# Optimization experiments

Measured on AMD Instinct MI355X. Metric: run time of the kernel, lower is better.

The kernel has to match this reference:

```python
import jax, jax.numpy as jnp
import numpy as np

N_NODES = 100000
N_EDGES = 1600000
N_ETYPES = 3
IN_FEATS = 128
HEADS = 4
OUT_FEATS = 16
EDGE_FEATS = 64
NEG_SLOPE = 0.2


def setup_inputs() -> dict:
    key = jax.random.key(0)
    ks = jax.random.split(key, 10)
    return {
        "x": jax.random.normal(ks[0], (N_NODES, IN_FEATS), jnp.float32),
        "W": jax.random.normal(ks[1], (IN_FEATS, HEADS * OUT_FEATS), jnp.float32) * 0.05,
        "W_e": jax.random.normal(ks[2], (EDGE_FEATS, HEADS * EDGE_FEATS), jnp.float32) * 0.05,
        "attn_l": jax.random.normal(ks[3], (HEADS, OUT_FEATS), jnp.float32) * 0.1,
        "attn_r": jax.random.normal(ks[4], (HEADS, OUT_FEATS), jnp.float32) * 0.1,
        "attn_e": jax.random.normal(ks[5], (HEADS, EDGE_FEATS), jnp.float32) * 0.1,
        "edge_emb": jax.random.normal(ks[6], (N_ETYPES, EDGE_FEATS), jnp.float32),
        "src": jax.random.randint(ks[7], (N_EDGES,), 0, N_NODES, jnp.int32),
        "dst": jax.random.randint(ks[8], (N_EDGES,), 0, N_NODES, jnp.int32),
        "etype": jax.random.randint(ks[9], (N_EDGES,), 0, N_ETYPES, jnp.int32),
    }


def reference(x, W, W_e, attn_l, attn_r, attn_e, edge_emb, src, dst, etype):
    N = x.shape[0]
    H, D = attn_l.shape
    # node projection: [N, H, D]
    feat = (x @ W).reshape(N, H, D)
    # per-node attention halves: [N, H]
    el = jnp.einsum("nhd,hd->nh", feat, attn_l)
    er = jnp.einsum("nhd,hd->nh", feat, attn_r)
    # per-etype edge term: [T, H]
    e_feat = (edge_emb @ W_e).reshape(edge_emb.shape[0], H, -1)
    ee = jnp.einsum("the,he->th", e_feat, attn_e)
    # per-edge pre-softmax score: [E, H]
    s = el[src] + er[dst] + ee[etype]
    s = jnp.where(s > 0, s, NEG_SLOPE * s)  # leaky_relu
    # edge softmax over incoming edges of each dst node (homogeneous graph)
    m = jax.ops.segment_max(s, dst, num_segments=N)
    e = jnp.exp(s - m[dst])
    z = jax.ops.segment_sum(e, dst, num_segments=N)
    a = e / z[dst]  # [E, H]
    # u_mul_e + sum aggregation: [N, H, D]
    msg = feat[src] * a[:, :, None]
    rst = jax.ops.segment_sum(msg, dst, num_segments=N)
    return rst, a
```

## Files before the change

kernel.cpp:

```cpp
#include <hip/hip_runtime.h>
#include <hip/hip_bf16.h>

#define N_NODES   100000
#define N_EDGES   1600000
#define N_ETYPES  3
#define IN_FEATS  128
#define HEADS     4
#define OUT_FEATS 16
#define EDGE_FEATS 64
#define HD        64
#define NEG_SLOPE 0.2f
#define MAXD_LDS  128

#define NBUCK     800
#define NPB       125
#define PBLK      400
#define EPB       4000
#define BCAP      2560
#define FROWS     32
#define NFEAT     (N_NODES / FROWS)
#define WTROWS    80


typedef short s16x8 __attribute__((ext_vector_type(8)));
typedef float f32x4 __attribute__((ext_vector_type(4)));

__device__ __forceinline__ short f2bs(float f) {
    __hip_bfloat16 h = __float2bfloat16(f);
    return *reinterpret_cast<short*>(&h);
}

__global__ __launch_bounds__(256) void wt_prep_kernel(
    const float* __restrict__ W,
    const float* __restrict__ attn_l,
    const float* __restrict__ attn_r,
    short* __restrict__ WTb, int* __restrict__ cnt)
{
    const int t = blockIdx.x * 256 + threadIdx.x;
    const int n = t >> 7, k = t & 127;
    short v;
    if (n < 64) {
        v = f2bs(W[k * HD + n]);
    } else if (n < 72) {
        const int h = (n - 64) & 3;
        const float* av = (n < 68) ? attn_l : attn_r;
        float s = 0.f;
#pragma unroll
        for (int d = 0; d < OUT_FEATS; ++d)
            s += W[k * HD + h * OUT_FEATS + d] * av[h * OUT_FEATS + d];
        v = f2bs(s);
    } else {
        v = 0;
    }
    WTb[n * IN_FEATS + k] = v;
    if (blockIdx.x == 0)
        for (int j = threadIdx.x; j < NBUCK; j += 256) cnt[j] = 0;
}

#define XS_STRIDE 136
__global__ __launch_bounds__(320) void feat_scatter_kernel(
    const float* __restrict__ x,
    const short* __restrict__ WTb,
    const float* __restrict__ edge_emb,
    const float* __restrict__ W_e,
    const float* __restrict__ attn_e,
    const int* __restrict__ src, const int* __restrict__ dst,
    const int* __restrict__ etype,
    __hip_bfloat16* __restrict__ featb,
    float* __restrict__ el,
    float* __restrict__ er,
    float* __restrict__ ee,
    int* __restrict__ cnt, int2* __restrict__ sc_bucket)
{
    __shared__ __align__(16) char smem[FROWS * XS_STRIDE * 2];
    const int t = threadIdx.x;
    const int b = blockIdx.x;

    if (b < PBLK) {
        int* h = (int*)smem;
        int buld[13];
        for (int j = t; j < NBUCK; j += 320) h[j] = 0;
        __syncthreads();
        const int e0 = b * EPB;
        int k = 0;
        for (int i = t; i < EPB; i += 320, ++k) {
            const int dn = dst[e0 + i];
            const int bu = dn / NPB;
            const int ld = dn - bu * NPB;
            buld[k] = bu | (ld << 16);
            atomicAdd(&h[bu], 1);
        }
        __syncthreads();
        for (int j = t; j < NBUCK; j += 320) {
            const int c = h[j];
            h[j] = j * BCAP + (c ? atomicAdd(&cnt[j], c) : 0);
        }
        __syncthreads();
        k = 0;
        for (int i = t; i < EPB; i += 320, ++k) {
            const int e  = e0 + i;
            const int bu = buld[k] & 0xFFFF;
            const int ld = buld[k] >> 16;
            const int slot = atomicAdd(&h[bu], 1);
            sc_bucket[slot] = make_int2(src[e], e | (etype[e] << 21) | (ld << 23));
        }
        return;
    }

    if (b == PBLK) {
        const int wv = t >> 6, e = t & 63;
        for (int j = wv; j < N_ETYPES * HEADS; j += 5) {
            const int ty = j >> 2, h = j & 3;
            float ef = 0.f;
#pragma unroll
            for (int k = 0; k < EDGE_FEATS; ++k)
                ef += edge_emb[ty * EDGE_FEATS + k] *
                      W_e[k * (HEADS * EDGE_FEATS) + h * EDGE_FEATS + e];
            float v = ef * attn_e[h * EDGE_FEATS + e];
#pragma unroll
            for (int m = 1; m < 64; m <<= 1) v += __shfl_xor(v, m, 64);
            if (e == 0) ee[ty * HEADS + h] = v;
        }
        return;
    }

    short* Xs = (short*)smem;
    const int row0 = (b - PBLK - 1) * FROWS;
    if (t < 256) {
        const int r = t >> 3, k0 = (t & 7) * 16;
        const float4* xg = (const float4*)(x + (size_t)(row0 + r) * IN_FEATS + k0);
        const float4 v0 = xg[0], v1 = xg[1], v2 = xg[2], v3 = xg[3];
        s16x8 p0, p1;
        p0[0] = f2bs(v0.x); p0[1] = f2bs(v0.y); p0[2] = f2bs(v0.z); p0[3] = f2bs(v0.w);
        p0[4] = f2bs(v1.x); p0[5] = f2bs(v1.y); p0[6] = f2bs(v1.z); p0[7] = f2bs(v1.w);
        p1[0] = f2bs(v2.x); p1[1] = f2bs(v2.y); p1[2] = f2bs(v2.z); p1[3] = f2bs(v2.w);
        p1[4] = f2bs(v3.x); p1[5] = f2bs(v3.y); p1[6] = f2bs(v3.z); p1[7] = f2bs(v3.w);
        *(s16x8*)&Xs[r * XS_STRIDE + k0]     = p0;
        *(s16x8*)&Xs[r * XS_STRIDE + k0 + 8] = p1;
    }

    const int w    = t >> 6;
    const int lane = t & 63;
    const int m    = lane & 15;
    const int q    = lane >> 4;

    s16x8 bfr[4];
#pragma unroll
    for (int kb = 0; kb < 4; ++kb)
        bfr[kb] = *(const s16x8*)(WTb + (size_t)(w * 16 + m) * IN_FEATS + kb * 32 + q * 8);

    __syncthreads();

#pragma unroll
    for (int rg = 0; rg < 2; ++rg) {
        f32x4 acc = {0.f, 0.f, 0.f, 0.f};
#pragma unroll
        for (int kb = 0; kb < 4; ++kb) {
            const s16x8 af = *(const s16x8*)&Xs[(rg * 16 + m) * XS_STRIDE + kb * 32 + q * 8];
            acc = __builtin_amdgcn_mfma_f32_16x16x32_bf16(af, bfr[kb], acc, 0, 0, 0);
        }
        if (w < 4) {
#pragma unroll
            for (int r = 0; r < 4; ++r) {
                const int row = row0 + rg * 16 + q * 4 + r;
                featb[(size_t)row * HD + w * 16 + m] = __float2bfloat16(acc[r]);
            }
        } else {
#pragma unroll
            for (int r = 0; r < 4; ++r) {
                const int row = row0 + rg * 16 + q * 4 + r;
                if (m < 4)      el[row * HEADS + m]       = acc[r];
                else if (m < 8) er[row * HEADS + (m - 4)] = acc[r];
            }
        }
    }
}

__global__ __launch_bounds__(256) void bucket_csr_kernel(
    int2* __restrict__ sc_bucket, const int* __restrict__ cnt,
    int* __restrict__ ptr, int* __restrict__ deg)
{
    __shared__ int2 sbuf[BCAP];
    __shared__ int sdeg4[4][128];
    __shared__ int sdg[128];
    __shared__ int scur[128];
    const int t = threadIdx.x, b = blockIdx.x;
    const int wid = t >> 6;

    sdeg4[0][t & 127] = 0; sdeg4[1][t & 127] = 0;
    if (t < 128) { sdeg4[2][t] = 0; sdeg4[3][t] = 0; }
    __syncthreads();
    const int count = min(cnt[b], BCAP);
    const int base  = b * BCAP;

    for (int i = t; i < count; i += 256) {
        const int2 v = sc_bucket[base + i];
        sbuf[i] = v;
        atomicAdd(&sdeg4[wid][(v.y >> 23) & 0x7F], 1);
    }
    __syncthreads();
    int orig = 0;
    if (t < 128) {
        orig = sdeg4[0][t] + sdeg4[1][t] + sdeg4[2][t] + sdeg4[3][t];
        sdg[t] = orig;
    }
    __syncthreads();
    for (int off = 1; off < 128; off <<= 1) {
        const int v = (t < 128 && t >= off) ? sdg[t - off] : 0;
        __syncthreads();
        if (t < 128) sdg[t] += v;
        __syncthreads();
    }
    if (t < 128) {
        const int excl = sdg[t] - orig;
        if (t < NPB) {
            ptr[b * NPB + t] = base + excl;
            deg[b * NPB + t] = orig;
        }
        scur[t] = base + excl;
    }
    __syncthreads();
    for (int i = t; i < count; i += 256) {
        const int2 v = sbuf[i];
        const int ld = (v.y >> 23) & 0x7F;
        const int slot = atomicAdd(&scur[ld], 1);
        sc_bucket[slot] = make_int2(v.x, v.y & 0x7FFFFF);
    }
}

__global__ __launch_bounds__(256) void agg_kernel(
    const int2* __restrict__ sc_csr, const int* __restrict__ ptr,
    const int* __restrict__ deg_arr,
    const float* __restrict__ el, const float* __restrict__ er,
    const float* __restrict__ ee, const __hip_bfloat16* __restrict__ featb,
    float* __restrict__ rst, float* __restrict__ a_out)
{
    __shared__ float w_lds[4][MAXD_LDS * HEADS];
    __shared__ int   s_lds[4][MAXD_LDS];
    __shared__ int   e_lds[4][MAXD_LDS];
    const int wid  = threadIdx.x >> 6;
    const int lane = threadIdx.x & 63;
    const int n    = blockIdx.x * 4 + wid;

    const int p0  = ptr[n];
    const int deg = deg_arr[n];
    float* wl = w_lds[wid];
    int*   sl = s_lds[wid];
    int*   elds = e_lds[wid];
    const ushort* fb = (const ushort*)featb;

    if (deg <= MAXD_LDS) {
        const int eo = lane >> 2;
        const int hA = lane & 3;
        const float er_n = er[n * HEADS + hA];
        const float g0 = ee[hA], g1 = ee[HEADS + hA], g2 = ee[2 * HEADS + hA];

        float zacc = 0.f;
        for (int i0 = 0; i0 < deg; i0 += 32) {
            const int idxA = i0 + eo;
            const int idxB = i0 + 16 + eo;
            const bool pA = idxA < deg;
            const bool pB = idxB < deg;
            int2 vA = make_int2(0, 0), vB = make_int2(0, 0);
            if (pA) vA = sc_csr[p0 + idxA];
            if (pB) vB = sc_csr[p0 + idxB];
            float eA = 0.f, eB = 0.f;
            if (pA) eA = el[vA.x * HEADS + hA];
            if (pB) eB = el[vB.x * HEADS + hA];
            if (pA) {
                const int ty = vA.y >> 21;
                float s = eA + er_n + ((ty == 0) ? g0 : ((ty == 1) ? g1 : g2));
                s = s > 0.f ? s : NEG_SLOPE * s;
                const float w = __expf(s);
                wl[idxA * HEADS + hA] = w;
                if (hA == 0) sl[idxA] = vA.x;
                if (hA == 1) elds[idxA] = vA.y & 0x1FFFFF;
                zacc += w;
            }
            if (pB) {
                const int ty = vB.y >> 21;
                float s = eB + er_n + ((ty == 0) ? g0 : ((ty == 1) ? g1 : g2));
                s = s > 0.f ? s : NEG_SLOPE * s;
                const float w = __expf(s);
                wl[idxB * HEADS + hA] = w;
                if (hA == 0) sl[idxB] = vB.x;
                if (hA == 1) elds[idxB] = vB.y & 0x1FFFFF;
                zacc += w;
            }
        }
        zacc += __shfl_xor(zacc, 4, 64);
        zacc += __shfl_xor(zacc, 8, 64);
        zacc += __shfl_xor(zacc, 16, 64);
        zacc += __shfl_xor(zacc, 32, 64);
        const float izA = (deg > 0) ? __frcp_rn(zacc) : 0.f;

        for (int idx = eo; idx < deg; idx += 16)
            a_out[((size_t)elds[idx] << 2) + hA] = wl[idx * HEADS + hA] * izA;

        const int q8 = lane >> 3;
        const int c8 = lane & 7;
        const int h8 = c8 >> 1;
        const float inv_z = (deg > 0) ? __frcp_rn(__shfl(zacc, h8, 64)) : 0.f;

        float a0 = 0.f, a1 = 0.f, a2 = 0.f, a3 = 0.f;
        float a4 = 0.f, a5 = 0.f, a6 = 0.f, a7 = 0.f;
        int i = 0;
        for (; i + 16 <= deg; i += 16) {
            const int idxA = i + q8, idxB = i + 8 + q8;
            const int sA = sl[idxA], sB = sl[idxB];
            const float wA = wl[idxA * HEADS + h8];
            const float wB = wl[idxB * HEADS + h8];
            const uint4 fA = *(const uint4*)(fb + ((size_t)sA << 6) + (c8 << 3));
            const uint4 fB = *(const uint4*)(fb + ((size_t)sB << 6) + (c8 << 3));
            a0 += __uint_as_float(fA.x << 16) * wA;
            a1 += __uint_as_float(fA.x & 0xFFFF0000u) * wA;
            a2 += __uint_as_float(fA.y << 16) * wA;
            a3 += __uint_as_float(fA.y & 0xFFFF0000u) * wA;
            a4 += __uint_as_float(fA.z << 16) * wA;
            a5 += __uint_as_float(fA.z & 0xFFFF0000u) * wA;
            a6 += __uint_as_float(fA.w << 16) * wA;
            a7 += __uint_as_float(fA.w & 0xFFFF0000u) * wA;
            a0 += __uint_as_float(fB.x << 16) * wB;
            a1 += __uint_as_float(fB.x & 0xFFFF0000u) * wB;
            a2 += __uint_as_float(fB.y << 16) * wB;
            a3 += __uint_as_float(fB.y & 0xFFFF0000u) * wB;
            a4 += __uint_as_float(fB.z << 16) * wB;
            a5 += __uint_as_float(fB.z & 0xFFFF0000u) * wB;
            a6 += __uint_as_float(fB.w << 16) * wB;
            a7 += __uint_as_float(fB.w & 0xFFFF0000u) * wB;
        }
        if (i + 8 <= deg) {
            const int idx = i + q8;
            const int sA = sl[idx];
            const float wA = wl[idx * HEADS + h8];
            const uint4 fA = *(const uint4*)(fb + ((size_t)sA << 6) + (c8 << 3));
            a0 += __uint_as_float(fA.x << 16) * wA;
            a1 += __uint_as_float(fA.x & 0xFFFF0000u) * wA;
            a2 += __uint_as_float(fA.y << 16) * wA;
            a3 += __uint_as_float(fA.y & 0xFFFF0000u) * wA;
            a4 += __uint_as_float(fA.z << 16) * wA;
            a5 += __uint_as_float(fA.z & 0xFFFF0000u) * wA;
            a6 += __uint_as_float(fA.w << 16) * wA;
            a7 += __uint_as_float(fA.w & 0xFFFF0000u) * wA;
            i += 8;
        }
        if (i + q8 < deg) {
            const int idx = i + q8;
            const int sA = sl[idx];
            const float wA = wl[idx * HEADS + h8];
            const uint4 fA = *(const uint4*)(fb + ((size_t)sA << 6) + (c8 << 3));
            a0 += __uint_as_float(fA.x << 16) * wA;
            a1 += __uint_as_float(fA.x & 0xFFFF0000u) * wA;
            a2 += __uint_as_float(fA.y << 16) * wA;
            a3 += __uint_as_float(fA.y & 0xFFFF0000u) * wA;
            a4 += __uint_as_float(fA.z << 16) * wA;
            a5 += __uint_as_float(fA.z & 0xFFFF0000u) * wA;
            a6 += __uint_as_float(fA.w << 16) * wA;
            a7 += __uint_as_float(fA.w & 0xFFFF0000u) * wA;
        }
        a0 += __shfl_xor(a0, 8, 64); a0 += __shfl_xor(a0, 16, 64); a0 += __shfl_xor(a0, 32, 64);
        a1 += __shfl_xor(a1, 8, 64); a1 += __shfl_xor(a1, 16, 64); a1 += __shfl_xor(a1, 32, 64);
        a2 += __shfl_xor(a2, 8, 64); a2 += __shfl_xor(a2, 16, 64); a2 += __shfl_xor(a2, 32, 64);
        a3 += __shfl_xor(a3, 8, 64); a3 += __shfl_xor(a3, 16, 64); a3 += __shfl_xor(a3, 32, 64);
        a4 += __shfl_xor(a4, 8, 64); a4 += __shfl_xor(a4, 16, 64); a4 += __shfl_xor(a4, 32, 64);
        a5 += __shfl_xor(a5, 8, 64); a5 += __shfl_xor(a5, 16, 64); a5 += __shfl_xor(a5, 32, 64);
        a6 += __shfl_xor(a6, 8, 64); a6 += __shfl_xor(a6, 16, 64); a6 += __shfl_xor(a6, 32, 64);
        a7 += __shfl_xor(a7, 8, 64); a7 += __shfl_xor(a7, 16, 64); a7 += __shfl_xor(a7, 32, 64);
        if (q8 == 0) {
            f32x4 v0 = {a0 * inv_z, a1 * inv_z, a2 * inv_z, a3 * inv_z};
            f32x4 v1 = {a4 * inv_z, a5 * inv_z, a6 * inv_z, a7 * inv_z};
            *(f32x4*)(rst + (size_t)n * HD + (c8 << 3))     = v0;
            *(f32x4*)(rst + (size_t)n * HD + (c8 << 3) + 4) = v1;
        }
    } else {
        const int hA = lane & 3;
        const int eo = lane >> 2;
        const float er_nA = er[n * HEADS + hA];
        const float b0 = ee[hA], b1 = ee[HEADS + hA], b2 = ee[2 * HEADS + hA];
        float zacc = 0.f;
        for (int base = 0; base < deg; base += 16) {
            const int idx = base + eo;
            if (idx < deg) {
                const int2 v = sc_csr[p0 + idx];
                const int ty = v.y >> 21;
                float s = el[v.x * HEADS + hA] + er_nA + ((ty == 0) ? b0 : ((ty == 1) ? b1 : b2));
                s = s > 0.f ? s : NEG_SLOPE * s;
                zacc += __expf(s);
            }
        }
#pragma unroll
        for (int m = 4; m < 64; m <<= 1) zacc += __shfl_xor(zacc, m, 64);
        const int h = lane >> 4;
        const int d = lane & 15;
        const float inv_z = __frcp_rn(__shfl(zacc, h, 64));
        const float er_n = er[n * HEADS + h];
        const float g0 = ee[h], g1 = ee[HEADS + h], g2 = ee[2 * HEADS + h];
        float racc = 0.f;
        for (int i = 0; i < deg; ++i) {
            const int2 v = sc_csr[p0 + i];
            const int ty = v.y >> 21;
            float s = el[v.x * HEADS + h] + er_n + ((ty == 0) ? g0 : ((ty == 1) ? g1 : g2));
            s = s > 0.f ? s : NEG_SLOPE * s;
            const float a = __expf(s) * inv_z;
            racc += __bfloat162float(featb[(size_t)v.x * HD + lane]) * a;
            if (d == 0) a_out[((size_t)(v.y & 0x1FFFFF) << 2) + h] = a;
        }
        rst[(size_t)n * HD + lane] = racc;
    }
}

extern "C" void kernel_launch(void* const* d_in, const int* in_sizes, int n_in,
                              void* d_out, int out_size, void* d_ws, size_t ws_size,
                              hipStream_t stream)
{
    const float* x        = (const float*)d_in[0];
    const float* W        = (const float*)d_in[1];
    const float* W_e      = (const float*)d_in[2];
    const float* attn_l   = (const float*)d_in[3];
    const float* attn_r   = (const float*)d_in[4];
    const float* attn_e   = (const float*)d_in[5];
    const float* edge_emb = (const float*)d_in[6];
    const int* src   = (const int*)d_in[7];
    const int* dst   = (const int*)d_in[8];
    const int* etype = (const int*)d_in[9];

    float* out     = (float*)d_out;
    float* rst_out = out;
    float* a_out   = out + (size_t)N_NODES * HD;

    char* w = (char*)d_ws;
    __hip_bfloat16* featb = (__hip_bfloat16*)w; w += (size_t)N_NODES * HD * 2;
    float* el    = (float*)w;  w += (size_t)N_NODES * HEADS * 4;
    float* er    = (float*)w;  w += (size_t)N_NODES * HEADS * 4;
    float* ee    = (float*)w;  w += 64;
    int*   ptr   = (int*)w;    w += (size_t)(N_NODES + 8) * 4;
    int*   deg   = (int*)w;    w += (size_t)(N_NODES + 8) * 4;
    int*   cnt   = (int*)w;    w += (size_t)(NBUCK + 8) * 4;
    short* WTb   = (short*)w;  w += (size_t)WTROWS * IN_FEATS * 2;
    int2*  sc_bucket = (int2*)w; w += ((size_t)NBUCK * BCAP + 2048) * 8;

    wt_prep_kernel<<<(WTROWS * IN_FEATS) / 256, 256, 0, stream>>>(
        W, attn_l, attn_r, WTb, cnt);

    feat_scatter_kernel<<<PBLK + 1 + NFEAT, 320, 0, stream>>>(
        x, WTb, edge_emb, W_e, attn_e,
        src, dst, etype, featb, el, er, ee, cnt, sc_bucket);

    bucket_csr_kernel<<<NBUCK, 256, 0, stream>>>(sc_bucket, cnt, ptr, deg);

    agg_kernel<<<N_NODES / 4, 256, 0, stream>>>(
        sc_bucket, ptr, deg, el, er, ee, featb, rst_out, a_out);
}
```

Baseline: 246.3 us.

## Fuse bucket CSR sort into aggregation kernel using LDS-resident sorted edges

Merges the bucket counting-sort kernel and the per-node aggregation kernel into one. Each bucket is sorted in shared memory and then aggregated directly from there, with two blocks per bucket that each redo the sort and then handle half of the bucket's nodes. This drops the global write-back of the sorted edges, the ptr/deg arrays and one kernel launch. The cost is duplicated sorting work, fewer and heavier blocks (1600 instead of 25000), and more LDS per block, which can lower occupancy for the latency-bound gather loop.

```diff
diff --git a/kernel.cpp b/kernel.cpp
--- a/kernel.cpp
+++ b/kernel.cpp
@@ -176,16 +176,24 @@
     }
 }
 
-__global__ __launch_bounds__(256) void bucket_csr_kernel(
-    int2* __restrict__ sc_bucket, const int* __restrict__ cnt,
-    int* __restrict__ ptr, int* __restrict__ deg)
+__global__ __launch_bounds__(256) void bucket_agg_kernel(
+    const int2* __restrict__ sc_bucket, const int* __restrict__ cnt,
+    const float* __restrict__ el, const float* __restrict__ er,
+    const float* __restrict__ ee, const __hip_bfloat16* __restrict__ featb,
+    float* __restrict__ rst, float* __restrict__ a_out)
 {
-    __shared__ int2 sbuf[BCAP];
-    __shared__ int sdeg4[4][128];
-    __shared__ int sdg[128];
-    __shared__ int scur[128];
-    const int t = threadIdx.x, b = blockIdx.x;
-    const int wid = t >> 6;
+    __shared__ int2  ssort[BCAP];
+    __shared__ int   sdeg4[4][128];
+    __shared__ int   sdg[128];
+    __shared__ int   soff[128];
+    __shared__ int   scur[128];
+    __shared__ float w_lds[4][MAXD_LDS * HEADS];
+    const int t    = threadIdx.x;
+    const int bb   = blockIdx.x;
+    const int b    = bb >> 1;
+    const int half = bb & 1;
+    const int wid  = t >> 6;
+    const int lane = t & 63;
 
     sdeg4[0][t & 127] = 0; sdeg4[1][t & 127] = 0;
     if (t < 128) { sdeg4[2][t] = 0; sdeg4[3][t] = 0; }
@@ -193,11 +201,8 @@
     const int count = min(cnt[b], BCAP);
     const int base  = b * BCAP;
 
-    for (int i = t; i < count; i += 256) {
-        const int2 v = sc_bucket[base + i];
-        sbuf[i] = v;
-        atomicAdd(&sdeg4[wid][(v.y >> 23) & 0x7F], 1);
-    }
+    for (int i = t; i < count; i += 256)
+        atomicAdd(&sdeg4[wid][(sc_bucket[base + i].y >> 23) & 0x7F], 1);
     __syncthreads();
     int orig = 0;
     if (t < 128) {
@@ -213,199 +218,187 @@
     }
     if (t < 128) {
         const int excl = sdg[t] - orig;
-        if (t < NPB) {
-            ptr[b * NPB + t] = base + excl;
-            deg[b * NPB + t] = orig;
-        }
-        scur[t] = base + excl;
+        soff[t] = excl;
+        scur[t] = excl;
+        sdg[t]  = orig;
     }
     __syncthreads();
     for (int i = t; i < count; i += 256) {
-        const int2 v = sbuf[i];
+        const int2 v = sc_bucket[base + i];
         const int ld = (v.y >> 23) & 0x7F;
         const int slot = atomicAdd(&scur[ld], 1);
-        sc_bucket[slot] = make_int2(v.x, v.y & 0x7FFFFF);
-    }
-}
-
-__global__ __launch_bounds__(256) void agg_kernel(
-    const int2* __restrict__ sc_csr, const int* __restrict__ ptr,
-    const int* __restrict__ deg_arr,
-    const float* __restrict__ el, const float* __restrict__ er,
-    const float* __restrict__ ee, const __hip_bfloat16* __restrict__ featb,
-    float* __restrict__ rst, float* __restrict__ a_out)
-{
-    __shared__ float w_lds[4][MAXD_LDS * HEADS];
-    __shared__ int   s_lds[4][MAXD_LDS];
-    __shared__ int   e_lds[4][MAXD_LDS];
-    const int wid  = threadIdx.x >> 6;
-    const int lane = threadIdx.x & 63;
-    const int n    = blockIdx.x * 4 + wid;
-
-    const int p0  = ptr[n];
-    const int deg = deg_arr[n];
-    float* wl = w_lds[wid];
-    int*   sl = s_lds[wid];
-    int*   elds = e_lds[wid];
+        ssort[slot] = make_int2(v.x, v.y & 0x7FFFFF);
+    }
+    __syncthreads();
+
+    const int ln0 = half ? 63 : 0;
+    const int ln1 = half ? NPB : 63;
     const ushort* fb = (const ushort*)featb;
 
-    if (deg <= MAXD_LDS) {
-        const int eo = lane >> 2;
-        const int hA = lane & 3;
-        const float er_n = er[n * HEADS + hA];
-        const float g0 = ee[hA], g1 = ee[HEADS + hA], g2 = ee[2 * HEADS + hA];
-
-        float zacc = 0.f;
-        for (int i0 = 0; i0 < deg; i0 += 32) {
-            const int idxA = i0 + eo;
-            const int idxB = i0 + 16 + eo;
-            const bool pA = idxA < deg;
-            const bool pB = idxB < deg;
-            int2 vA = make_int2(0, 0), vB = make_int2(0, 0);
-            if (pA) vA = sc_csr[p0 + idxA];
-            if (pB) vB = sc_csr[p0 + idxB];
-            float eA = 0.f, eB = 0.f;
-            if (pA) eA = el[vA.x * HEADS + hA];
-            if (pB) eB = el[vB.x * HEADS + hA];
-            if (pA) {
-                const int ty = vA.y >> 21;
-                float s = eA + er_n + ((ty == 0) ? g0 : ((ty == 1) ? g1 : g2));
+    for (int ln = ln0 + wid; ln < ln1; ln += 4) {
+        const int n   = b * NPB + ln;
+        const int p0  = soff[ln];
+        const int deg = sdg[ln];
+        float* wl = w_lds[wid];
+
+        if (deg <= MAXD_LDS) {
+            const int eo = lane >> 2;
+            const int hA = lane & 3;
+            const float er_n = er[n * HEADS + hA];
+            const float g0 = ee[hA], g1 = ee[HEADS + hA], g2 = ee[2 * HEADS + hA];
+
+            float zacc = 0.f;
+            for (int i0 = 0; i0 < deg; i0 += 32) {
+                const int idxA = i0 + eo;
+                const int idxB = i0 + 16 + eo;
+                const bool pA = idxA < deg;
+                const bool pB = idxB < deg;
+                int2 vA = make_int2(0, 0), vB = make_int2(0, 0);
+                if (pA) vA = ssort[p0 + idxA];
+                if (pB) vB = ssort[p0 + idxB];
+                float eA = 0.f, eB = 0.f;
+                if (pA) eA = el[vA.x * HEADS + hA];
+                if (pB) eB = el[vB.x * HEADS + hA];
+                if (pA) {
+                    const int ty = vA.y >> 21;
+                    float s = eA + er_n + ((ty == 0) ? g0 : ((ty == 1) ? g1 : g2));
+                    s = s > 0.f ? s : NEG_SLOPE * s;
+                    const float w = __expf(s);
+                    wl[idxA * HEADS + hA] = w;
+                    zacc += w;
+                }
+                if (pB) {
+                    const int ty = vB.y >> 21;
+                    float s = eB + er_n + ((ty == 0) ? g0 : ((ty == 1) ? g1 : g2));
+                    s = s > 0.f ? s : NEG_SLOPE * s;
+                    const float w = __expf(s);
+                    wl[idxB * HEADS + hA] = w;
+                    zacc += w;
+                }
+            }
+            zacc += __shfl_xor(zacc, 4, 64);
+            zacc += __shfl_xor(zacc, 8, 64);
+            zacc += __shfl_xor(zacc, 16, 64);
+            zacc += __shfl_xor(zacc, 32, 64);
+            const float izA = (deg > 0) ? __frcp_rn(zacc) : 0.f;
+
+            for (int idx = eo; idx < deg; idx += 16)
+                a_out[((size_t)(ssort[p0 + idx].y & 0x1FFFFF) << 2) + hA] =
+                    wl[idx * HEADS + hA] * izA;
+
+            const int q8 = lane >> 3;
+            const int c8 = lane & 7;
+            const int h8 = c8 >> 1;
+            const float inv_z = (deg > 0) ? __frcp_rn(__shfl(zacc, h8, 64)) : 0.f;
+
+            float a0 = 0.f, a1 = 0.f, a2 = 0.f, a3 = 0.f;
+            float a4 = 0.f, a5 = 0.f, a6 = 0.f, a7 = 0.f;
+            int i = 0;
+            for (; i + 16 <= deg; i += 16) {
+                const int idxA = i + q8, idxB = i + 8 + q8;
+                const int sA = ssort[p0 + idxA].x;
+                const int sB = ssort[p0 + idxB].x;
+                const float wA = wl[idxA * HEADS + h8];
+                const float wB = wl[idxB * HEADS + h8];
+                const uint4 fA = *(const uint4*)(fb + ((size_t)sA << 6) + (c8 << 3));
+                const uint4 fB = *(const uint4*)(fb + ((size_t)sB << 6) + (c8 << 3));
+                a0 += __uint_as_float(fA.x << 16) * wA;
+                a1 += __uint_as_float(fA.x & 0xFFFF0000u) * wA;
+                a2 += __uint_as_float(fA.y << 16) * wA;
+                a3 += __uint_as_float(fA.y & 0xFFFF0000u) * wA;
+                a4 += __uint_as_float(fA.z << 16) * wA;
+                a5 += __uint_as_float(fA.z & 0xFFFF0000u) * wA;
+                a6 += __uint_as_float(fA.w << 16) * wA;
+                a7 += __uint_as_float(fA.w & 0xFFFF0000u) * wA;
+                a0 += __uint_as_float(fB.x << 16) * wB;
+                a1 += __uint_as_float(fB.x & 0xFFFF0000u) * wB;
+                a2 += __uint_as_float(fB.y << 16) * wB;
+                a3 += __uint_as_float(fB.y & 0xFFFF0000u) * wB;
+                a4 += __uint_as_float(fB.z << 16) * wB;
+                a5 += __uint_as_float(fB.z & 0xFFFF0000u) * wB;
+                a6 += __uint_as_float(fB.w << 16) * wB;
+                a7 += __uint_as_float(fB.w & 0xFFFF0000u) * wB;
+            }
+            if (i + 8 <= deg) {
+                const int idx = i + q8;
+                const int sA = ssort[p0 + idx].x;
+                const float wA = wl[idx * HEADS + h8];
+                const uint4 fA = *(const uint4*)(fb + ((size_t)sA << 6) + (c8 << 3));
+                a0 += __uint_as_float(fA.x << 16) * wA;
+                a1 += __uint_as_float(fA.x & 0xFFFF0000u) * wA;
+                a2 += __uint_as_float(fA.y << 16) * wA;
+                a3 += __uint_as_float(fA.y & 0xFFFF0000u) * wA;
+                a4 += __uint_as_float(fA.z << 16) * wA;
+                a5 += __uint_as_float(fA.z & 0xFFFF0000u) * wA;
+                a6 += __uint_as_float(fA.w << 16) * wA;
+                a7 += __uint_as_float(fA.w & 0xFFFF0000u) * wA;
+                i += 8;
+            }
+            if (i + q8 < deg) {
+                const int idx = i + q8;
+                const int sA = ssort[p0 + idx].x;
+                const float wA = wl[idx * HEADS + h8];
+                const uint4 fA = *(const uint4*)(fb + ((size_t)sA << 6) + (c8 << 3));
+                a0 += __uint_as_float(fA.x << 16) * wA;
+                a1 += __uint_as_float(fA.x & 0xFFFF0000u) * wA;
+                a2 += __uint_as_float(fA.y << 16) * wA;
+                a3 += __uint_as_float(fA.y & 0xFFFF0000u) * wA;
+                a4 += __uint_as_float(fA.z << 16) * wA;
+                a5 += __uint_as_float(fA.z & 0xFFFF0000u) * wA;
+                a6 += __uint_as_float(fA.w << 16) * wA;
+                a7 += __uint_as_float(fA.w & 0xFFFF0000u) * wA;
+            }
+            a0 += __shfl_xor(a0, 8, 64); a0 += __shfl_xor(a0, 16, 64); a0 += __shfl_xor(a0, 32, 64);
+            a1 += __shfl_xor(a1, 8, 64); a1 += __shfl_xor(a1, 16, 64); a1 += __shfl_xor(a1, 32, 64);
+            a2 += __shfl_xor(a2, 8, 64); a2 += __shfl_xor(a2, 16, 64); a2 += __shfl_xor(a2, 32, 64);
+            a3 += __shfl_xor(a3, 8, 64); a3 += __shfl_xor(a3, 16, 64); a3 += __shfl_xor(a3, 32, 64);
+            a4 += __shfl_xor(a4, 8, 64); a4 += __shfl_xor(a4, 16, 64); a4 += __shfl_xor(a4, 32, 64);
+            a5 += __shfl_xor(a5, 8, 64); a5 += __shfl_xor(a5, 16, 64); a5 += __shfl_xor(a5, 32, 64);
+            a6 += __shfl_xor(a6, 8, 64); a6 += __shfl_xor(a6, 16, 64); a6 += __shfl_xor(a6, 32, 64);
+            a7 += __shfl_xor(a7, 8, 64); a7 += __shfl_xor(a7, 16, 64); a7 += __shfl_xor(a7, 32, 64);
+            if (q8 == 0) {
+                f32x4 v0 = {a0 * inv_z, a1 * inv_z, a2 * inv_z, a3 * inv_z};
+                f32x4 v1 = {a4 * inv_z, a5 * inv_z, a6 * inv_z, a7 * inv_z};
+                *(f32x4*)(rst + (size_t)n * HD + (c8 << 3))     = v0;
+                *(f32x4*)(rst + (size_t)n * HD + (c8 << 3) + 4) = v1;
+            }
+        } else {
+            const int hA = lane & 3;
+            const int eo = lane >> 2;
+            const float er_nA = er[n * HEADS + hA];
+            const float b0 = ee[hA], b1 = ee[HEADS + hA], b2 = ee[2 * HEADS + hA];
+            float zacc = 0.f;
+            for (int bs = 0; bs < deg; bs += 16) {
+                const int idx = bs + eo;
+                if (idx < deg) {
+                    const int2 v = ssort[p0 + idx];
+                    const int ty = v.y >> 21;
+                    float s = el[v.x * HEADS + hA] + er_nA +
+                              ((ty == 0) ? b0 : ((ty == 1) ? b1 : b2));
+                    s = s > 0.f ? s : NEG_SLOPE * s;
+                    zacc += __expf(s);
+                }
+            }
+#pragma unroll
+            for (int m = 4; m < 64; m <<= 1) zacc += __shfl_xor(zacc, m, 64);
+            const int h = lane >> 4;
+            const int d = lane & 15;
+            const float inv_z = __frcp_rn(__shfl(zacc, h, 64));
+            const float er_n = er[n * HEADS + h];
+            const float g0 = ee[h], g1 = ee[HEADS + h], g2 = ee[2 * HEADS + h];
+            float racc = 0.f;
+            for (int i = 0; i < deg; ++i) {
+                const int2 v = ssort[p0 + i];
+                const int ty = v.y >> 21;
+                float s = el[v.x * HEADS + h] + er_n +
+                          ((ty == 0) ? g0 : ((ty == 1) ? g1 : g2));
                 s = s > 0.f ? s : NEG_SLOPE * s;
-                const float w = __expf(s);
-                wl[idxA * HEADS + hA] = w;
-                if (hA == 0) sl[idxA] = vA.x;
-                if (hA == 1) elds[idxA] = vA.y & 0x1FFFFF;
-                zacc += w;
-            }
-            if (pB) {
-                const int ty = vB.y >> 21;
-                float s = eB + er_n + ((ty == 0) ? g0 : ((ty == 1) ? g1 : g2));
-                s = s > 0.f ? s : NEG_SLOPE * s;
-                const float w = __expf(s);
-                wl[idxB * HEADS + hA] = w;
-                if (hA == 0) sl[idxB] = vB.x;
-                if (hA == 1) elds[idxB] = vB.y & 0x1FFFFF;
-                zacc += w;
-            }
-        }
-        zacc += __shfl_xor(zacc, 4, 64);
-        zacc += __shfl_xor(zacc, 8, 64);
-        zacc += __shfl_xor(zacc, 16, 64);
-        zacc += __shfl_xor(zacc, 32, 64);
-        const float izA = (deg > 0) ? __frcp_rn(zacc) : 0.f;
-
-        for (int idx = eo; idx < deg; idx += 16)
-            a_out[((size_t)elds[idx] << 2) + hA] = wl[idx * HEADS + hA] * izA;
-
-        const int q8 = lane >> 3;
-        const int c8 = lane & 7;
-        const int h8 = c8 >> 1;
-        const float inv_z = (deg > 0) ? __frcp_rn(__shfl(zacc, h8, 64)) : 0.f;
-
-        float a0 = 0.f, a1 = 0.f, a2 = 0.f, a3 = 0.f;
-        float a4 = 0.f, a5 = 0.f, a6 = 0.f, a7 = 0.f;
-        int i = 0;
-        for (; i + 16 <= deg; i += 16) {
-            const int idxA = i + q8, idxB = i + 8 + q8;
-            const int sA = sl[idxA], sB = sl[idxB];
-            const float wA = wl[idxA * HEADS + h8];
-            const float wB = wl[idxB * HEADS + h8];
-            const uint4 fA = *(const uint4*)(fb + ((size_t)sA << 6) + (c8 << 3));
-            const uint4 fB = *(const uint4*)(fb + ((size_t)sB << 6) + (c8 << 3));
-            a0 += __uint_as_float(fA.x << 16) * wA;
-            a1 += __uint_as_float(fA.x & 0xFFFF0000u) * wA;
-            a2 += __uint_as_float(fA.y << 16) * wA;
-            a3 += __uint_as_float(fA.y & 0xFFFF0000u) * wA;
-            a4 += __uint_as_float(fA.z << 16) * wA;
-            a5 += __uint_as_float(fA.z & 0xFFFF0000u) * wA;
-            a6 += __uint_as_float(fA.w << 16) * wA;
-            a7 += __uint_as_float(fA.w & 0xFFFF0000u) * wA;
-            a0 += __uint_as_float(fB.x << 16) * wB;
-            a1 += __uint_as_float(fB.x & 0xFFFF0000u) * wB;
-            a2 += __uint_as_float(fB.y << 16) * wB;
-            a3 += __uint_as_float(fB.y & 0xFFFF0000u) * wB;
-            a4 += __uint_as_float(fB.z << 16) * wB;
-            a5 += __uint_as_float(fB.z & 0xFFFF0000u) * wB;
-            a6 += __uint_as_float(fB.w << 16) * wB;
-            a7 += __uint_as_float(fB.w & 0xFFFF0000u) * wB;
-        }
-        if (i + 8 <= deg) {
-            const int idx = i + q8;
-            const int sA = sl[idx];
-            const float wA = wl[idx * HEADS + h8];
-            const uint4 fA = *(const uint4*)(fb + ((size_t)sA << 6) + (c8 << 3));
-            a0 += __uint_as_float(fA.x << 16) * wA;
-            a1 += __uint_as_float(fA.x & 0xFFFF0000u) * wA;
-            a2 += __uint_as_float(fA.y << 16) * wA;
-            a3 += __uint_as_float(fA.y & 0xFFFF0000u) * wA;
-            a4 += __uint_as_float(fA.z << 16) * wA;
-            a5 += __uint_as_float(fA.z & 0xFFFF0000u) * wA;
-            a6 += __uint_as_float(fA.w << 16) * wA;
-            a7 += __uint_as_float(fA.w & 0xFFFF0000u) * wA;
-            i += 8;
-        }
-        if (i + q8 < deg) {
-            const int idx = i + q8;
-            const int sA = sl[idx];
-            const float wA = wl[idx * HEADS + h8];
-            const uint4 fA = *(const uint4*)(fb + ((size_t)sA << 6) + (c8 << 3));
-            a0 += __uint_as_float(fA.x << 16) * wA;
-            a1 += __uint_as_float(fA.x & 0xFFFF0000u) * wA;
-            a2 += __uint_as_float(fA.y << 16) * wA;
-            a3 += __uint_as_float(fA.y & 0xFFFF0000u) * wA;
-            a4 += __uint_as_float(fA.z << 16) * wA;
-            a5 += __uint_as_float(fA.z & 0xFFFF0000u) * wA;
-            a6 += __uint_as_float(fA.w << 16) * wA;
-            a7 += __uint_as_float(fA.w & 0xFFFF0000u) * wA;
-        }
-        a0 += __shfl_xor(a0, 8, 64); a0 += __shfl_xor(a0, 16, 64); a0 += __shfl_xor(a0, 32, 64);
-        a1 += __shfl_xor(a1, 8, 64); a1 += __shfl_xor(a1, 16, 64); a1 += __shfl_xor(a1, 32, 64);
-        a2 += __shfl_xor(a2, 8, 64); a2 += __shfl_xor(a2, 16, 64); a2 += __shfl_xor(a2, 32, 64);
-        a3 += __shfl_xor(a3, 8, 64); a3 += __shfl_xor(a3, 16, 64); a3 += __shfl_xor(a3, 32, 64);
-        a4 += __shfl_xor(a4, 8, 64); a4 += __shfl_xor(a4, 16, 64); a4 += __shfl_xor(a4, 32, 64);
-        a5 += __shfl_xor(a5, 8, 64); a5 += __shfl_xor(a5, 16, 64); a5 += __shfl_xor(a5, 32, 64);
-        a6 += __shfl_xor(a6, 8, 64); a6 += __shfl_xor(a6, 16, 64); a6 += __shfl_xor(a6, 32, 64);
-        a7 += __shfl_xor(a7, 8, 64); a7 += __shfl_xor(a7, 16, 64); a7 += __shfl_xor(a7, 32, 64);
-        if (q8 == 0) {
-            f32x4 v0 = {a0 * inv_z, a1 * inv_z, a2 * inv_z, a3 * inv_z};
-            f32x4 v1 = {a4 * inv_z, a5 * inv_z, a6 * inv_z, a7 * inv_z};
-            *(f32x4*)(rst + (size_t)n * HD + (c8 << 3))     = v0;
-            *(f32x4*)(rst + (size_t)n * HD + (c8 << 3) + 4) = v1;
-        }
-    } else {
-        const int hA = lane & 3;
-        const int eo = lane >> 2;
-        const float er_nA = er[n * HEADS + hA];
-        const float b0 = ee[hA], b1 = ee[HEADS + hA], b2 = ee[2 * HEADS + hA];
-        float zacc = 0.f;
-        for (int base = 0; base < deg; base += 16) {
-            const int idx = base + eo;
-            if (idx < deg) {
-                const int2 v = sc_csr[p0 + idx];
-                const int ty = v.y >> 21;
-                float s = el[v.x * HEADS + hA] + er_nA + ((ty == 0) ? b0 : ((ty == 1) ? b1 : b2));
-                s = s > 0.f ? s : NEG_SLOPE * s;
-                zacc += __expf(s);
-            }
-        }
-#pragma unroll
-        for (int m = 4; m < 64; m <<= 1) zacc += __shfl_xor(zacc, m, 64);
-        const int h = lane >> 4;
-        const int d = lane & 15;
-        const float inv_z = __frcp_rn(__shfl(zacc, h, 64));
-        const float er_n = er[n * HEADS + h];
-        const float g0 = ee[h], g1 = ee[HEADS + h], g2 = ee[2 * HEADS + h];
-        float racc = 0.f;
-        for (int i = 0; i < deg; ++i) {
-            const int2 v = sc_csr[p0 + i];
-            const int ty = v.y >> 21;
-            float s = el[v.x * HEADS + h] + er_n + ((ty == 0) ? g0 : ((ty == 1) ? g1 : g2));
-            s = s > 0.f ? s : NEG_SLOPE * s;
-            const float a = __expf(s) * inv_z;
-            racc += __bfloat162float(featb[(size_t)v.x * HD + lane]) * a;
-            if (d == 0) a_out[((size_t)(v.y & 0x1FFFFF) << 2) + h] = a;
-        }
-        rst[(size_t)n * HD + lane] = racc;
+                const float a = __expf(s) * inv_z;
+                racc += __bfloat162float(featb[(size_t)v.x * HD + lane]) * a;
+                if (d == 0) a_out[((size_t)(v.y & 0x1FFFFF) << 2) + h] = a;
+            }
+            rst[(size_t)n * HD + lane] = racc;
+        }
     }
 }
 
@@ -433,8 +426,6 @@
     float* el    = (float*)w;  w += (size_t)N_NODES * HEADS * 4;
     float* er    = (float*)w;  w += (size_t)N_NODES * HEADS * 4;
     float* ee    = (float*)w;  w += 64;
-    int*   ptr   = (int*)w;    w += (size_t)(N_NODES + 8) * 4;
-    int*   deg   = (int*)w;    w += (size_t)(N_NODES + 8) * 4;
     int*   cnt   = (int*)w;    w += (size_t)(NBUCK + 8) * 4;
     short* WTb   = (short*)w;  w += (size_t)WTROWS * IN_FEATS * 2;
     int2*  sc_bucket = (int2*)w; w += ((size_t)NBUCK * BCAP + 2048) * 8;
@@ -446,8 +437,6 @@
         x, WTb, edge_emb, W_e, attn_e,
         src, dst, etype, featb, el, er, ee, cnt, sc_bucket);
 
-    bucket_csr_kernel<<<NBUCK, 256, 0, stream>>>(sc_bucket, cnt, ptr, deg);
-
-    agg_kernel<<<N_NODES / 4, 256, 0, stream>>>(
-        sc_bucket, ptr, deg, el, er, ee, featb, rst_out, a_out);
+    bucket_agg_kernel<<<2 * NBUCK, 256, 0, stream>>>(
+        sc_bucket, cnt, el, er, ee, featb, rst_out, a_out);
 }
```

After: 284.2 us. +15.4%, slower.
